# Kernel tuning notes

Measured on AMD Instinct MI355X. Metric: run time of the kernel, lower is better.

Reference implementation:

```python
import jax, jax.numpy as jnp
import numpy as np

B, N, E = 8, 10000, 320000
IN_DIM, E_H, E_OUT, OUT_DIM = 16, 32, 32, 32
D_EDGE_IN = IN_DIM * 2 + 2 + 1  # src feats + tgt feats + edge_attr_norm(2) + edge_weight(1)


def setup_inputs() -> dict:
    key = jax.random.key(0)
    ks = jax.random.split(key, 10)
    x = jax.random.normal(ks[0], (B, N, IN_DIM), dtype=jnp.float32)
    edge_index = jax.random.randint(ks[1], (2, E), 0, N)
    # col 0 = city_dist (kept >= 0.5 to avoid divide-by-tiny), col 1 = city_direc
    edge_attr = jax.random.uniform(ks[2], (E, 2), dtype=jnp.float32) + 0.5
    wind_mean = jax.random.normal(ks[3], (2,), dtype=jnp.float32)
    wind_std = jax.random.uniform(ks[4], (2,), dtype=jnp.float32) + 0.5
    def lin(k, fo, fi):
        return jax.random.normal(k, (fo, fi), dtype=jnp.float32) / np.sqrt(fi).astype(np.float32)
    W1 = lin(ks[5], E_H, D_EDGE_IN); b1 = jnp.zeros((E_H,), jnp.float32)
    W2 = lin(ks[6], E_OUT, E_H);     b2 = jnp.zeros((E_OUT,), jnp.float32)
    W3 = lin(ks[7], OUT_DIM, E_OUT); b3 = jnp.zeros((OUT_DIM,), jnp.float32)
    return dict(x=x, edge_attr=edge_attr, wind_mean=wind_mean, wind_std=wind_std,
                W1=W1, b1=b1, W2=W2, b2=b2, W3=W3, b3=b3, edge_index=edge_index)


def reference(x, edge_attr, wind_mean, wind_std, W1, b1, W2, b2, W3, b3, edge_index):
    edge_src, edge_tgt = edge_index[0], edge_index[1]
    node_src = x[:, edge_src]   # [B, E, D] gather
    node_tgt = x[:, edge_tgt]   # [B, E, D]
    # de-normalize wind (last two feature channels of source node)
    src_wind = node_src[:, :, -2:] * wind_std[None, None, :] + wind_mean[None, None, :]
    src_wind_speed = src_wind[:, :, 0]
    src_wind_direc = src_wind[:, :, 1]
    city_dist = edge_attr[:, 0][None, :]   # [1, E]
    city_direc = edge_attr[:, 1][None, :]
    theta = jnp.abs(city_direc - src_wind_direc)                       # [B, E]
    edge_weight = jax.nn.relu(3.0 * src_wind_speed * jnp.cos(theta * 360.0 / 16.0) / city_dist)
    # normalization of edge_attr uses torch's unbiased std (ddof=1)
    ea_norm = (edge_attr - edge_attr.mean(axis=0)) / edge_attr.std(axis=0, ddof=1)  # [E, 2]
    feat = jnp.concatenate([
        node_src, node_tgt,
        jnp.broadcast_to(ea_norm[None], (node_src.shape[0], E, 2)),
        edge_weight[:, :, None],
    ], axis=-1)                                                        # [B, E, D_EDGE_IN]
    h = jax.nn.sigmoid(jnp.einsum('bef,hf->beh', feat, W1) + b1)       # edge MLP
    h = jax.nn.sigmoid(jnp.einsum('beh,oh->beo', h, W2) + b2)          # [B, E, E_OUT]
    agg = jnp.zeros((x.shape[0], x.shape[1], h.shape[-1]), h.dtype).at[:, edge_tgt].add(h)
    out = jax.nn.sigmoid(jnp.einsum('bno,po->bnp', agg, W3) + b3)      # node MLP -> [B, N, OUT_DIM]
    return out
```

## Files before the change

kernel.cpp:

```cpp
#include <hip/hip_runtime.h>
#include <hip/hip_fp16.h>
#include <cmath>

constexpr int Bc = 8;
constexpr int Nn = 10000;
constexpr int Ec = 320000;
constexpr int IN = 16;
constexpr int EH = 32;
constexpr int EO = 32;
constexpr int OD = 32;

constexpr size_t U_CNT = 8;
constexpr size_t U_CUR = U_CNT + Nn;
constexpr size_t U_REC = 20016;
constexpr size_t U_PA  = U_REC + 4 * (size_t)Ec;
constexpr size_t U_PB  = U_PA + (size_t)Bc * Nn * 16;
constexpr size_t U_PW  = U_PB + (size_t)Bc * Nn * 16;

constexpr int HIST_BLOCKS = 256;
constexpr int PRE_BLOCKS  = (Bc * Nn + 255) / 256;
constexpr int ZERO_BLOCKS = 512;

constexpr int WPW = 1408;

typedef _Float16 f16x8 __attribute__((ext_vector_type(8)));
typedef float f32x4 __attribute__((ext_vector_type(4)));

__device__ __forceinline__ float sigmoid_f(float x) {
    return __builtin_amdgcn_rcpf(1.0f + __expf(-x));
}
__device__ __forceinline__ unsigned pkh(float lo, float hi) {
    return __builtin_bit_cast(unsigned, __builtin_amdgcn_cvt_pkrtz(lo, hi));
}

__global__ __launch_bounds__(256) void prep_kernel(
    const float* __restrict__ ea, const int* __restrict__ ei,
    const float* __restrict__ x, const float* __restrict__ wmean,
    const float* __restrict__ wstd, const float* __restrict__ W1,
    const float* __restrict__ b1, float* __restrict__ ws,
    float* __restrict__ out)
{
    const int blk = blockIdx.x;
    const int tid = threadIdx.x;

    if (blk < HIST_BLOCKS) {
        int* cnt = (int*)ws + U_CNT;
        const int lo = blk * (Ec / HIST_BLOCKS);
        const int hi = lo + (Ec / HIST_BLOCKS);
        float s0 = 0.f, s1 = 0.f, q0 = 0.f, q1 = 0.f;
        for (int i = lo + tid; i < hi; i += 256) {
            float2 v = reinterpret_cast<const float2*>(ea)[i];
            s0 += v.x; s1 += v.y; q0 += v.x * v.x; q1 += v.y * v.y;
            atomicAdd(&cnt[ei[Ec + i]], 1);
        }
#pragma unroll
        for (int off = 32; off > 0; off >>= 1) {
            s0 += __shfl_down(s0, off);
            s1 += __shfl_down(s1, off);
            q0 += __shfl_down(q0, off);
            q1 += __shfl_down(q1, off);
        }
        if ((tid & 63) == 0) {
            atomicAdd(&ws[0], s0);
            atomicAdd(&ws[1], s1);
            atomicAdd(&ws[2], q0);
            atomicAdd(&ws[3], q1);
        }
    } else if (blk < HIST_BLOCKS + PRE_BLOCKS) {
        const int idx = (blk - HIST_BLOCKS) * 256 + tid;
        if (idx >= Bc * Nn) return;
        const float4* xr = reinterpret_cast<const float4*>(x + (size_t)idx * IN);
        float xv[16];
        float4 t;
        t = xr[0]; xv[0]  = t.x; xv[1]  = t.y; xv[2]  = t.z; xv[3]  = t.w;
        t = xr[1]; xv[4]  = t.x; xv[5]  = t.y; xv[6]  = t.z; xv[7]  = t.w;
        t = xr[2]; xv[8]  = t.x; xv[9]  = t.y; xv[10] = t.z; xv[11] = t.w;
        t = xr[3]; xv[12] = t.x; xv[13] = t.y; xv[14] = t.z; xv[15] = t.w;

        __half2* PA = reinterpret_cast<__half2*>((unsigned*)ws + U_PA) + (size_t)idx * 16;
        __half2* PB = reinterpret_cast<__half2*>((unsigned*)ws + U_PB) + (size_t)idx * 16;
#pragma unroll
        for (int p = 0; p < 16; ++p) {
            float a[2], bb[2];
#pragma unroll
            for (int j = 0; j < 2; ++j) {
                const int o = 2 * p + j;
                const float* wr = W1 + o * 35;
                float av = 0.f, bv = b1[o];
#pragma unroll
                for (int f = 0; f < 16; ++f) {
                    av += xv[f] * wr[f];
                    bv += xv[f] * wr[16 + f];
                }
                a[j] = av; bb[j] = bv;
            }
            PA[p] = __half2{__float2half(a[0]), __float2half(a[1])};
            PB[p] = __half2{__float2half(bb[0]), __float2half(bb[1])};
        }
        float2* PW = reinterpret_cast<float2*>((unsigned*)ws + U_PW);
        PW[idx] = make_float2(3.0f * (xv[14] * wstd[0] + wmean[0]),
                              xv[15] * wstd[1] + wmean[1]);
    } else {
        float4* o4 = reinterpret_cast<float4*>(out);
        constexpr int TOT4 = Bc * Nn * 32 / 4;
        const float4 z = make_float4(0.f, 0.f, 0.f, 0.f);
        for (int i = (blk - HIST_BLOCKS - PRE_BLOCKS) * 256 + tid; i < TOT4;
             i += ZERO_BLOCKS * 256)
            o4[i] = z;
    }
}

__global__ __launch_bounds__(1024) void scan_kernel(float* __restrict__ ws) {
    const int tid = threadIdx.x;
    const int lane = tid & 63;
    const int w = tid >> 6;
    if (tid == 0) {
        float s0 = ws[0], s1 = ws[1], q0 = ws[2], q1 = ws[3];
        float m0 = s0 / (float)Ec, m1 = s1 / (float)Ec;
        float v0 = (q0 - s0 * m0) / (float)(Ec - 1);
        float v1 = (q1 - s1 * m1) / (float)(Ec - 1);
        ws[4] = m0; ws[5] = m1;
        ws[6] = rsqrtf(v0); ws[7] = rsqrtf(v1);
    }
    int* cnt    = (int*)ws + U_CNT;
    int* cursor = (int*)ws + U_CUR;

    constexpr int PER = 10;
    const int lo = tid * PER;
    int local[PER];
    int sum = 0;
#pragma unroll
    for (int k = 0; k < PER; ++k) {
        const int i = lo + k;
        const int c = (i < Nn) ? cnt[i] : 0;
        local[k] = sum;
        sum += c;
    }
    int v = sum;
#pragma unroll
    for (int off = 1; off < 64; off <<= 1) {
        int u = __shfl_up(v, off);
        if (lane >= off) v += u;
    }
    __shared__ int wt[16];
    __shared__ int woff[16];
    if (lane == 63) wt[w] = v;
    __syncthreads();
    if (w == 0) {
        int t = (lane < 16) ? wt[lane] : 0;
        int tv = t;
#pragma unroll
        for (int off = 1; off < 16; off <<= 1) {
            int u = __shfl_up(tv, off);
            if (lane >= off) tv += u;
        }
        if (lane < 16) woff[lane] = tv - t;
    }
    __syncthreads();
    const int base = woff[w] + (v - sum);
#pragma unroll
    for (int k = 0; k < PER; ++k) {
        const int i = lo + k;
        if (i < Nn) cursor[i] = base + local[k];
    }
}

__global__ __launch_bounds__(256) void record_kernel(const int* __restrict__ ei,
                                                     const float* __restrict__ ea,
                                                     float* __restrict__ ws) {
    int* cursor = (int*)ws + U_CUR;
    uint4* rec  = reinterpret_cast<uint4*>((unsigned*)ws + U_REC);
    const int e = blockIdx.x * 256 + threadIdx.x;
    const int src = ei[e];
    const int tgt = ei[Ec + e];
    const float2 v = reinterpret_cast<const float2*>(ea)[e];
    const int pos = atomicAdd(&cursor[tgt], 1);
    rec[pos] = make_uint4((unsigned)src, (unsigned)tgt,
                          __builtin_bit_cast(unsigned, v.x),
                          __builtin_bit_cast(unsigned, v.y));
}

__global__ __launch_bounds__(256, 7) void edge_kernel(
    const float* __restrict__ W1, const float* __restrict__ W2,
    const float* __restrict__ b2, const float* __restrict__ ws,
    float* __restrict__ agg)
{
    __shared__ unsigned lds[4 * WPW];
    const int tid  = threadIdx.x;
    const int lane = tid & 63;
    const int wid  = tid >> 6;
    unsigned* wl = lds + wid * WPW;

    const int bid = blockIdx.x;
    const int b   = bid & 7;
    const int gid = (bid >> 3) * 256 + wid * 64 + lane;

    const unsigned* wsu = (const unsigned*)ws;
    const uint4 rec = reinterpret_cast<const uint4*>(wsu + U_REC)[gid];
    const int src = (int)rec.x;
    const int tgt = (int)rec.y;
    const float eax = __builtin_bit_cast(float, rec.z);
    const float eay = __builtin_bit_cast(float, rec.w);

    const float2 pw = reinterpret_cast<const float2*>(wsu + U_PW)[b * Nn + src];
    const float theta = fabsf(eay - pw.y);
    const float ewt = fmaxf(pw.x * __cosf(theta * 22.5f) * __builtin_amdgcn_rcpf(eax), 0.0f);
    const float f32v = (eax - ws[4]) * ws[6];
    const float f33v = (eay - ws[5]) * ws[7];

    const uint4* pa4 = reinterpret_cast<const uint4*>(wsu + U_PA + ((size_t)b * Nn + src) * 16);
    const uint4* pb4 = reinterpret_cast<const uint4*>(wsu + U_PB + ((size_t)b * Nn + tgt) * 16);

    unsigned hw[16];
#pragma unroll
    for (int q = 0; q < 4; ++q) {
        const uint4 ua = pa4[q];
        const uint4 ub = pb4[q];
        const unsigned au[4] = {ua.x, ua.y, ua.z, ua.w};
        const unsigned bu[4] = {ub.x, ub.y, ub.z, ub.w};
#pragma unroll
        for (int j = 0; j < 4; ++j) {
            const int p = 4 * q + j;
            const __half2 s = __hadd2(__builtin_bit_cast(__half2, au[j]),
                                      __builtin_bit_cast(__half2, bu[j]));
            const float2 f = __half22float2(s);
            const int o0 = 2 * p, o1 = 2 * p + 1;
            const float acc0 = f.x + f32v * W1[o0 * 35 + 32]
                                   + f33v * W1[o0 * 35 + 33]
                                   + ewt  * W1[o0 * 35 + 34];
            const float acc1 = f.y + f32v * W1[o1 * 35 + 32]
                                   + f33v * W1[o1 * 35 + 33]
                                   + ewt  * W1[o1 * 35 + 34];
            hw[p] = pkh(sigmoid_f(acc0), sigmoid_f(acc1));
        }
    }
    {
        uint4* hrow = reinterpret_cast<uint4*>(wl + lane * 20);
#pragma unroll
        for (int q = 0; q < 4; ++q)
            hrow[q] = make_uint4(hw[4*q], hw[4*q+1], hw[4*q+2], hw[4*q+3]);
    }

    const int tprev = __shfl_up(tgt, 1);
    const bool head = (lane == 0) || (tprev != tgt);
    const unsigned long long mask = __ballot(head);
    const unsigned long long mle = (~0ULL) >> (63 - lane);
    const int run = __popcll(mask & mle) - 1;
    const int nruns = __popcll(mask);
    wl[1280 + lane] = (unsigned)run;
    if (head) wl[1344 + run] = (unsigned)tgt;

    const int c16 = lane & 15;
    const int hq  = lane >> 4;

    f16x8 bw[2];
#pragma unroll
    for (int t = 0; t < 2; ++t) {
        const float* wr = W2 + (c16 + 16 * t) * 32 + 8 * hq;
        const float4 w0 = *reinterpret_cast<const float4*>(wr);
        const float4 w1 = *reinterpret_cast<const float4*>(wr + 4);
        const uint4 pk = make_uint4(pkh(w0.x, w0.y), pkh(w0.z, w0.w),
                                    pkh(w1.x, w1.y), pkh(w1.z, w1.w));
        bw[t] = __builtin_bit_cast(f16x8, pk);
    }

    f32x4 c[4][2];
#pragma unroll
    for (int m = 0; m < 4; ++m) {
        const uint4 av = *reinterpret_cast<const uint4*>(wl + (16 * m + c16) * 20 + 4 * hq);
        const f16x8 afr = __builtin_bit_cast(f16x8, av);
#pragma unroll
        for (int t = 0; t < 2; ++t) {
            f32x4 z = {0.f, 0.f, 0.f, 0.f};
            c[m][t] = __builtin_amdgcn_mfma_f32_16x16x32_f16(afr, bw[t], z, 0, 0, 0);
        }
    }

    __builtin_amdgcn_sched_barrier(0);
    asm volatile("s_waitcnt lgkmcnt(0)" ::: "memory");
    __builtin_amdgcn_sched_barrier(0);

    const float b2v[2] = { b2[c16], b2[c16 + 16] };
#pragma unroll
    for (int m = 0; m < 4; ++m) {
#pragma unroll
        for (int t = 0; t < 2; ++t) {
            const float v0 = sigmoid_f(c[m][t][0] + b2v[t]);
            const float v1 = sigmoid_f(c[m][t][1] + b2v[t]);
            const float v2 = sigmoid_f(c[m][t][2] + b2v[t]);
            const float v3 = sigmoid_f(c[m][t][3] + b2v[t]);
            const uint2 pk = make_uint2(pkh(v0, v1), pkh(v2, v3));
            *reinterpret_cast<uint2*>(wl + (c16 + 16 * t) * 36 + 8 * m + 2 * hq) = pk;
        }
    }

    f16x8 vb[2][2];
    unsigned rid[2][8];
#pragma unroll
    for (int kk = 0; kk < 2; ++kk) {
#pragma unroll
        for (int t = 0; t < 2; ++t) {
            const uint4 vv = *reinterpret_cast<const uint4*>(wl + (c16 + 16 * t) * 36 + 16 * kk + 4 * hq);
            vb[kk][t] = __builtin_bit_cast(f16x8, vv);
        }
        const uint4 r0 = *reinterpret_cast<const uint4*>(wl + 1280 + 32 * kk + 8 * hq);
        const uint4 r1 = *reinterpret_cast<const uint4*>(wl + 1280 + 32 * kk + 8 * hq + 4);
        rid[kk][0] = r0.x; rid[kk][1] = r0.y; rid[kk][2] = r0.z; rid[kk][3] = r0.w;
        rid[kk][4] = r1.x; rid[kk][5] = r1.y; rid[kk][6] = r1.z; rid[kk][7] = r1.w;
    }

    const int nm = (nruns + 15) >> 4;
    for (int mr = 0; mr < nm; ++mr) {
        const unsigned rowg = (unsigned)(16 * mr + c16);
        f32x4 d0 = {0.f, 0.f, 0.f, 0.f};
        f32x4 d1 = {0.f, 0.f, 0.f, 0.f};
#pragma unroll
        for (int kk = 0; kk < 2; ++kk) {
            unsigned iw[4];
#pragma unroll
            for (int w = 0; w < 4; ++w) {
                iw[w] = (rid[kk][2 * w]     == rowg ? 0x3C00u : 0u)
                      | (rid[kk][2 * w + 1] == rowg ? 0x3C000000u : 0u);
            }
            const f16x8 ifr = __builtin_bit_cast(f16x8, make_uint4(iw[0], iw[1], iw[2], iw[3]));
            d0 = __builtin_amdgcn_mfma_f32_16x16x32_f16(ifr, vb[kk][0], d0, 0, 0, 0);
            d1 = __builtin_amdgcn_mfma_f32_16x16x32_f16(ifr, vb[kk][1], d1, 0, 0, 0);
        }
#pragma unroll
        for (int r = 0; r < 4; ++r) {
            const int rn = 16 * mr + 4 * hq + r;
            const unsigned tr = wl[1344 + (rn & 63)];
            if (rn < nruns) {
                float* dst = agg + ((size_t)b * Nn + tr) * 32;
                atomicAdd(dst + c16,      d0[r]);
                atomicAdd(dst + c16 + 16, d1[r]);
            }
        }
    }
}

__global__ __launch_bounds__(256) void node_kernel(
    const float* __restrict__ W3, const float* __restrict__ b3,
    float* __restrict__ out)
{
    const int idx = blockIdx.x * 256 + threadIdx.x;
    if (idx >= Bc * Nn) return;
    float* row = out + (size_t)idx * OD;

    float a[EO];
#pragma unroll
    for (int i = 0; i < EO / 4; ++i) {
        float4 t = reinterpret_cast<float4*>(row)[i];
        a[4 * i] = t.x; a[4 * i + 1] = t.y; a[4 * i + 2] = t.z; a[4 * i + 3] = t.w;
    }
    float r[OD];
#pragma unroll
    for (int p = 0; p < OD; ++p) {
        const float* wr = W3 + p * EO;
        float s = b3[p];
#pragma unroll
        for (int o = 0; o < EO; ++o) s += a[o] * wr[o];
        r[p] = sigmoid_f(s);
    }
#pragma unroll
    for (int i = 0; i < OD / 4; ++i) {
        float4 t;
        t.x = r[4 * i + 0]; t.y = r[4 * i + 1];
        t.z = r[4 * i + 2]; t.w = r[4 * i + 3];
        reinterpret_cast<float4*>(row)[i] = t;
    }
}

extern "C" void kernel_launch(void* const* d_in, const int* in_sizes, int n_in,
                              void* d_out, int out_size, void* d_ws, size_t ws_size,
                              hipStream_t stream) {
    const float* x     = (const float*)d_in[0];
    const float* ea    = (const float*)d_in[1];
    const float* wmean = (const float*)d_in[2];
    const float* wstd  = (const float*)d_in[3];
    const float* W1    = (const float*)d_in[4];
    const float* b1    = (const float*)d_in[5];
    const float* W2    = (const float*)d_in[6];
    const float* b2    = (const float*)d_in[7];
    const float* W3    = (const float*)d_in[8];
    const float* b3    = (const float*)d_in[9];
    const int*   ei    = (const int*)d_in[10];
    float* out = (float*)d_out;
    float* ws  = (float*)d_ws;

    hipMemsetAsync(d_ws, 0, (U_CNT + Nn) * sizeof(float), stream);

    prep_kernel<<<HIST_BLOCKS + PRE_BLOCKS + ZERO_BLOCKS, 256, 0, stream>>>(
        ea, ei, x, wmean, wstd, W1, b1, ws, out);
    scan_kernel<<<1, 1024, 0, stream>>>(ws);
    record_kernel<<<Ec / 256, 256, 0, stream>>>(ei, ea, ws);
    edge_kernel<<<(Ec / 256) * Bc, 256, 0, stream>>>(W1, W2, b2, ws, out);
    node_kernel<<<(Bc * Nn + 255) / 256, 256, 0, stream>>>(W3, b3, out);
}
```

Before: 195.5 us.

## Process two batches per edge block and fold exp scaling into weights

The edge kernel now handles two batch indices per block, looping over them. This reuses the edge record load, run/segment detection, edge-attr normalization and W2 fragment setup across batches and halves the grid size. Separately, -log2(e) is pre-folded into the precomputed PA/PB projections, the normalization scales, the W2 fragments and b2, so the sigmoid can use a raw exp2 instead of expf. The trade-off is fewer blocks in flight and a serialized per-block loop. Pre-scaling in fp16 also slightly changes rounding.

```diff
diff --git a/kernel.cpp b/kernel.cpp
--- a/kernel.cpp
+++ b/kernel.cpp
@@ -10,6 +10,8 @@
 constexpr int EO = 32;
 constexpr int OD = 32;
 
+constexpr float S2 = -1.44269504f;
+
 constexpr size_t U_CNT = 8;
 constexpr size_t U_CUR = U_CNT + Nn;
 constexpr size_t U_REC = 20016;
@@ -20,6 +22,7 @@
 constexpr int HIST_BLOCKS = 256;
 constexpr int PRE_BLOCKS  = (Bc * Nn + 255) / 256;
 constexpr int ZERO_BLOCKS = 512;
+constexpr int TILES = Ec / 256;
 
 constexpr int WPW = 1408;
 
@@ -28,6 +31,9 @@
 
 __device__ __forceinline__ float sigmoid_f(float x) {
     return __builtin_amdgcn_rcpf(1.0f + __expf(-x));
+}
+__device__ __forceinline__ float sig_s(float xs) {
+    return __builtin_amdgcn_rcpf(1.0f + __builtin_amdgcn_exp2f(xs));
 }
 __device__ __forceinline__ unsigned pkh(float lo, float hi) {
     return __builtin_bit_cast(unsigned, __builtin_amdgcn_cvt_pkrtz(lo, hi));
@@ -77,8 +83,8 @@
         t = xr[2]; xv[8]  = t.x; xv[9]  = t.y; xv[10] = t.z; xv[11] = t.w;
         t = xr[3]; xv[12] = t.x; xv[13] = t.y; xv[14] = t.z; xv[15] = t.w;
 
-        __half2* PA = reinterpret_cast<__half2*>((unsigned*)ws + U_PA) + (size_t)idx * 16;
-        __half2* PB = reinterpret_cast<__half2*>((unsigned*)ws + U_PB) + (size_t)idx * 16;
+        unsigned* PA = (unsigned*)ws + U_PA + (size_t)idx * 16;
+        unsigned* PB = (unsigned*)ws + U_PB + (size_t)idx * 16;
 #pragma unroll
         for (int p = 0; p < 16; ++p) {
             float a[2], bb[2];
@@ -92,10 +98,10 @@
                     av += xv[f] * wr[f];
                     bv += xv[f] * wr[16 + f];
                 }
-                a[j] = av; bb[j] = bv;
-            }
-            PA[p] = __half2{__float2half(a[0]), __float2half(a[1])};
-            PB[p] = __half2{__float2half(bb[0]), __float2half(bb[1])};
+                a[j] = av * S2; bb[j] = bv * S2;
+            }
+            PA[p] = pkh(a[0], a[1]);
+            PB[p] = pkh(bb[0], bb[1]);
         }
         float2* PW = reinterpret_cast<float2*>((unsigned*)ws + U_PW);
         PW[idx] = make_float2(3.0f * (xv[14] * wstd[0] + wmean[0]),
@@ -120,7 +126,7 @@
         float v0 = (q0 - s0 * m0) / (float)(Ec - 1);
         float v1 = (q1 - s1 * m1) / (float)(Ec - 1);
         ws[4] = m0; ws[5] = m1;
-        ws[6] = rsqrtf(v0); ws[7] = rsqrtf(v1);
+        ws[6] = S2 * rsqrtf(v0); ws[7] = S2 * rsqrtf(v1);
     }
     int* cnt    = (int*)ws + U_CNT;
     int* cursor = (int*)ws + U_CUR;
@@ -191,9 +197,10 @@
     const int wid  = tid >> 6;
     unsigned* wl = lds + wid * WPW;
 
-    const int bid = blockIdx.x;
-    const int b   = bid & 7;
-    const int gid = (bid >> 3) * 256 + wid * 64 + lane;
+    const int bid  = blockIdx.x;
+    const int cls  = bid & 3;
+    const int tile = bid >> 2;
+    const int gid  = tile * 256 + wid * 64 + lane;
 
     const unsigned* wsu = (const unsigned*)ws;
     const uint4 rec = reinterpret_cast<const uint4*>(wsu + U_REC)[gid];
@@ -202,44 +209,8 @@
     const float eax = __builtin_bit_cast(float, rec.z);
     const float eay = __builtin_bit_cast(float, rec.w);
 
-    const float2 pw = reinterpret_cast<const float2*>(wsu + U_PW)[b * Nn + src];
-    const float theta = fabsf(eay - pw.y);
-    const float ewt = fmaxf(pw.x * __cosf(theta * 22.5f) * __builtin_amdgcn_rcpf(eax), 0.0f);
     const float f32v = (eax - ws[4]) * ws[6];
     const float f33v = (eay - ws[5]) * ws[7];
-
-    const uint4* pa4 = reinterpret_cast<const uint4*>(wsu + U_PA + ((size_t)b * Nn + src) * 16);
-    const uint4* pb4 = reinterpret_cast<const uint4*>(wsu + U_PB + ((size_t)b * Nn + tgt) * 16);
-
-    unsigned hw[16];
-#pragma unroll
-    for (int q = 0; q < 4; ++q) {
-        const uint4 ua = pa4[q];
-        const uint4 ub = pb4[q];
-        const unsigned au[4] = {ua.x, ua.y, ua.z, ua.w};
-        const unsigned bu[4] = {ub.x, ub.y, ub.z, ub.w};
-#pragma unroll
-        for (int j = 0; j < 4; ++j) {
-            const int p = 4 * q + j;
-            const __half2 s = __hadd2(__builtin_bit_cast(__half2, au[j]),
-                                      __builtin_bit_cast(__half2, bu[j]));
-            const float2 f = __half22float2(s);
-            const int o0 = 2 * p, o1 = 2 * p + 1;
-            const float acc0 = f.x + f32v * W1[o0 * 35 + 32]
-                                   + f33v * W1[o0 * 35 + 33]
-                                   + ewt  * W1[o0 * 35 + 34];
-            const float acc1 = f.y + f32v * W1[o1 * 35 + 32]
-                                   + f33v * W1[o1 * 35 + 33]
-                                   + ewt  * W1[o1 * 35 + 34];
-            hw[p] = pkh(sigmoid_f(acc0), sigmoid_f(acc1));
-        }
-    }
-    {
-        uint4* hrow = reinterpret_cast<uint4*>(wl + lane * 20);
-#pragma unroll
-        for (int q = 0; q < 4; ++q)
-            hrow[q] = make_uint4(hw[4*q], hw[4*q+1], hw[4*q+2], hw[4*q+3]);
-    }
 
     const int tprev = __shfl_up(tgt, 1);
     const bool head = (lane == 0) || (tprev != tgt);
@@ -259,81 +230,128 @@
         const float* wr = W2 + (c16 + 16 * t) * 32 + 8 * hq;
         const float4 w0 = *reinterpret_cast<const float4*>(wr);
         const float4 w1 = *reinterpret_cast<const float4*>(wr + 4);
-        const uint4 pk = make_uint4(pkh(w0.x, w0.y), pkh(w0.z, w0.w),
-                                    pkh(w1.x, w1.y), pkh(w1.z, w1.w));
+        const uint4 pk = make_uint4(pkh(w0.x * S2, w0.y * S2), pkh(w0.z * S2, w0.w * S2),
+                                    pkh(w1.x * S2, w1.y * S2), pkh(w1.z * S2, w1.w * S2));
         bw[t] = __builtin_bit_cast(f16x8, pk);
     }
-
-    f32x4 c[4][2];
-#pragma unroll
-    for (int m = 0; m < 4; ++m) {
-        const uint4 av = *reinterpret_cast<const uint4*>(wl + (16 * m + c16) * 20 + 4 * hq);
-        const f16x8 afr = __builtin_bit_cast(f16x8, av);
-#pragma unroll
-        for (int t = 0; t < 2; ++t) {
-            f32x4 z = {0.f, 0.f, 0.f, 0.f};
-            c[m][t] = __builtin_amdgcn_mfma_f32_16x16x32_f16(afr, bw[t], z, 0, 0, 0);
-        }
-    }
-
-    __builtin_amdgcn_sched_barrier(0);
-    asm volatile("s_waitcnt lgkmcnt(0)" ::: "memory");
-    __builtin_amdgcn_sched_barrier(0);
-
-    const float b2v[2] = { b2[c16], b2[c16 + 16] };
-#pragma unroll
-    for (int m = 0; m < 4; ++m) {
-#pragma unroll
-        for (int t = 0; t < 2; ++t) {
-            const float v0 = sigmoid_f(c[m][t][0] + b2v[t]);
-            const float v1 = sigmoid_f(c[m][t][1] + b2v[t]);
-            const float v2 = sigmoid_f(c[m][t][2] + b2v[t]);
-            const float v3 = sigmoid_f(c[m][t][3] + b2v[t]);
-            const uint2 pk = make_uint2(pkh(v0, v1), pkh(v2, v3));
-            *reinterpret_cast<uint2*>(wl + (c16 + 16 * t) * 36 + 8 * m + 2 * hq) = pk;
-        }
-    }
-
-    f16x8 vb[2][2];
-    unsigned rid[2][8];
-#pragma unroll
-    for (int kk = 0; kk < 2; ++kk) {
-#pragma unroll
-        for (int t = 0; t < 2; ++t) {
-            const uint4 vv = *reinterpret_cast<const uint4*>(wl + (c16 + 16 * t) * 36 + 16 * kk + 4 * hq);
-            vb[kk][t] = __builtin_bit_cast(f16x8, vv);
-        }
-        const uint4 r0 = *reinterpret_cast<const uint4*>(wl + 1280 + 32 * kk + 8 * hq);
-        const uint4 r1 = *reinterpret_cast<const uint4*>(wl + 1280 + 32 * kk + 8 * hq + 4);
-        rid[kk][0] = r0.x; rid[kk][1] = r0.y; rid[kk][2] = r0.z; rid[kk][3] = r0.w;
-        rid[kk][4] = r1.x; rid[kk][5] = r1.y; rid[kk][6] = r1.z; rid[kk][7] = r1.w;
-    }
-
-    const int nm = (nruns + 15) >> 4;
-    for (int mr = 0; mr < nm; ++mr) {
-        const unsigned rowg = (unsigned)(16 * mr + c16);
-        f32x4 d0 = {0.f, 0.f, 0.f, 0.f};
-        f32x4 d1 = {0.f, 0.f, 0.f, 0.f};
+    const float b2v[2] = { b2[c16] * S2, b2[c16 + 16] * S2 };
+
+#pragma unroll 1
+    for (int bb = 0; bb < 2; ++bb) {
+        const int b = cls + 4 * bb;
+
+        __builtin_amdgcn_sched_barrier(0);
+        asm volatile("s_waitcnt lgkmcnt(0)" ::: "memory");
+        __builtin_amdgcn_sched_barrier(0);
+
+        const float2 pw = reinterpret_cast<const float2*>(wsu + U_PW)[b * Nn + src];
+        const float theta = fabsf(eay - pw.y);
+        const float ewtS = fmaxf(pw.x * __cosf(theta * 22.5f) * __builtin_amdgcn_rcpf(eax),
+                                 0.0f) * S2;
+
+        const uint4* pa4 = reinterpret_cast<const uint4*>(wsu + U_PA + ((size_t)b * Nn + src) * 16);
+        const uint4* pb4 = reinterpret_cast<const uint4*>(wsu + U_PB + ((size_t)b * Nn + tgt) * 16);
+
+        unsigned hw[16];
+#pragma unroll
+        for (int q = 0; q < 4; ++q) {
+            const uint4 ua = pa4[q];
+            const uint4 ub = pb4[q];
+            const unsigned au[4] = {ua.x, ua.y, ua.z, ua.w};
+            const unsigned bu[4] = {ub.x, ub.y, ub.z, ub.w};
+#pragma unroll
+            for (int j = 0; j < 4; ++j) {
+                const int p = 4 * q + j;
+                const __half2 s = __hadd2(__builtin_bit_cast(__half2, au[j]),
+                                          __builtin_bit_cast(__half2, bu[j]));
+                const float2 f = __half22float2(s);
+                const int o0 = 2 * p, o1 = 2 * p + 1;
+                const float acc0 = f.x + f32v * W1[o0 * 35 + 32]
+                                       + f33v * W1[o0 * 35 + 33]
+                                       + ewtS * W1[o0 * 35 + 34];
+                const float acc1 = f.y + f32v * W1[o1 * 35 + 32]
+                                       + f33v * W1[o1 * 35 + 33]
+                                       + ewtS * W1[o1 * 35 + 34];
+                hw[p] = pkh(sig_s(acc0), sig_s(acc1));
+            }
+        }
+        {
+            uint4* hrow = reinterpret_cast<uint4*>(wl + lane * 20);
+#pragma unroll
+            for (int q = 0; q < 4; ++q)
+                hrow[q] = make_uint4(hw[4*q], hw[4*q+1], hw[4*q+2], hw[4*q+3]);
+        }
+
+        f32x4 c[4][2];
+#pragma unroll
+        for (int m = 0; m < 4; ++m) {
+            const uint4 av = *reinterpret_cast<const uint4*>(wl + (16 * m + c16) * 20 + 4 * hq);
+            const f16x8 afr = __builtin_bit_cast(f16x8, av);
+#pragma unroll
+            for (int t = 0; t < 2; ++t) {
+                f32x4 z = {0.f, 0.f, 0.f, 0.f};
+                c[m][t] = __builtin_amdgcn_mfma_f32_16x16x32_f16(afr, bw[t], z, 0, 0, 0);
+            }
+        }
+
+        __builtin_amdgcn_sched_barrier(0);
+        asm volatile("s_waitcnt lgkmcnt(0)" ::: "memory");
+        __builtin_amdgcn_sched_barrier(0);
+
+#pragma unroll
+        for (int m = 0; m < 4; ++m) {
+#pragma unroll
+            for (int t = 0; t < 2; ++t) {
+                const float v0 = sig_s(c[m][t][0] + b2v[t]);
+                const float v1 = sig_s(c[m][t][1] + b2v[t]);
+                const float v2 = sig_s(c[m][t][2] + b2v[t]);
+                const float v3 = sig_s(c[m][t][3] + b2v[t]);
+                const uint2 pk = make_uint2(pkh(v0, v1), pkh(v2, v3));
+                *reinterpret_cast<uint2*>(wl + (c16 + 16 * t) * 36 + 8 * m + 2 * hq) = pk;
+            }
+        }
+
+        f16x8 vb[2][2];
+        unsigned rid[2][8];
 #pragma unroll
         for (int kk = 0; kk < 2; ++kk) {
-            unsigned iw[4];
-#pragma unroll
-            for (int w = 0; w < 4; ++w) {
-                iw[w] = (rid[kk][2 * w]     == rowg ? 0x3C00u : 0u)
-                      | (rid[kk][2 * w + 1] == rowg ? 0x3C000000u : 0u);
-            }
-            const f16x8 ifr = __builtin_bit_cast(f16x8, make_uint4(iw[0], iw[1], iw[2], iw[3]));
-            d0 = __builtin_amdgcn_mfma_f32_16x16x32_f16(ifr, vb[kk][0], d0, 0, 0, 0);
-            d1 = __builtin_amdgcn_mfma_f32_16x16x32_f16(ifr, vb[kk][1], d1, 0, 0, 0);
-        }
-#pragma unroll
-        for (int r = 0; r < 4; ++r) {
-            const int rn = 16 * mr + 4 * hq + r;
-            const unsigned tr = wl[1344 + (rn & 63)];
-            if (rn < nruns) {
-                float* dst = agg + ((size_t)b * Nn + tr) * 32;
-                atomicAdd(dst + c16,      d0[r]);
-                atomicAdd(dst + c16 + 16, d1[r]);
+#pragma unroll
+            for (int t = 0; t < 2; ++t) {
+                const uint4 vv = *reinterpret_cast<const uint4*>(wl + (c16 + 16 * t) * 36 + 16 * kk + 4 * hq);
+                vb[kk][t] = __builtin_bit_cast(f16x8, vv);
+            }
+            const uint4 r0 = *reinterpret_cast<const uint4*>(wl + 1280 + 32 * kk + 8 * hq);
+            const uint4 r1 = *reinterpret_cast<const uint4*>(wl + 1280 + 32 * kk + 8 * hq + 4);
+            rid[kk][0] = r0.x; rid[kk][1] = r0.y; rid[kk][2] = r0.z; rid[kk][3] = r0.w;
+            rid[kk][4] = r1.x; rid[kk][5] = r1.y; rid[kk][6] = r1.z; rid[kk][7] = r1.w;
+        }
+
+        const int nm = (nruns + 15) >> 4;
+        for (int mr = 0; mr < nm; ++mr) {
+            const unsigned rowg = (unsigned)(16 * mr + c16);
+            f32x4 d0 = {0.f, 0.f, 0.f, 0.f};
+            f32x4 d1 = {0.f, 0.f, 0.f, 0.f};
+#pragma unroll
+            for (int kk = 0; kk < 2; ++kk) {
+                unsigned iw[4];
+#pragma unroll
+                for (int w = 0; w < 4; ++w) {
+                    iw[w] = (rid[kk][2 * w]     == rowg ? 0x3C00u : 0u)
+                          | (rid[kk][2 * w + 1] == rowg ? 0x3C000000u : 0u);
+                }
+                const f16x8 ifr = __builtin_bit_cast(f16x8, make_uint4(iw[0], iw[1], iw[2], iw[3]));
+                d0 = __builtin_amdgcn_mfma_f32_16x16x32_f16(ifr, vb[kk][0], d0, 0, 0, 0);
+                d1 = __builtin_amdgcn_mfma_f32_16x16x32_f16(ifr, vb[kk][1], d1, 0, 0, 0);
+            }
+#pragma unroll
+            for (int r = 0; r < 4; ++r) {
+                const int rn = 16 * mr + 4 * hq + r;
+                const unsigned tr = wl[1344 + (rn & 63)];
+                if (rn < nruns) {
+                    float* dst = agg + ((size_t)b * Nn + tr) * 32;
+                    atomicAdd(dst + c16,      d0[r]);
+                    atomicAdd(dst + c16 + 16, d1[r]);
+                }
             }
         }
     }
@@ -394,6 +412,6 @@
         ea, ei, x, wmean, wstd, W1, b1, ws, out);
     scan_kernel<<<1, 1024, 0, stream>>>(ws);
     record_kernel<<<Ec / 256, 256, 0, stream>>>(ei, ea, ws);
-    edge_kernel<<<(Ec / 256) * Bc, 256, 0, stream>>>(W1, W2, b2, ws, out);
+    edge_kernel<<<TILES * 4, 256, 0, stream>>>(W1, W2, b2, ws, out);
     node_kernel<<<(Bc * Nn + 255) / 256, 256, 0, stream>>>(W3, b3, out);
 }
```

New measurement: 215.0 us. +9.9%, slower.
